# Optimization experiments

Hardware: AMD Instinct MI355X
Metric: run time of the kernel (lower is better)

The kernel has to match this reference:

```python
import jax, jax.numpy as jnp
import numpy as np

B, S, D = 2, 2048, 1024
H, DH = 16, 64  # n_heads, d_head; inner_dim = H*DH = 1024


def setup_inputs() -> dict:
    key = jax.random.key(0)
    ks = jax.random.split(key, 6)
    s = 0.02
    return {
        "query": jax.random.normal(ks[0], (B, S, D), jnp.float32),
        "context": jax.random.normal(ks[1], (B, S, D), jnp.float32),
        "Wq": jax.random.normal(ks[2], (D, H * DH), jnp.float32) * s,
        "Wk": jax.random.normal(ks[3], (D, H * DH), jnp.float32) * s,
        "Wv": jax.random.normal(ks[4], (D, H * DH), jnp.float32) * s,
        "Wo": jax.random.normal(ks[5], (H * DH, D), jnp.float32) * s,
        "bo": jnp.zeros((D,), jnp.float32),
    }


def reference(query, context, Wq, Wk, Wv, Wo, bo):
    scale = DH ** -0.5
    # projections -> [B, H, S, DH]
    q = (query @ Wq).reshape(B, S, H, DH).transpose(0, 2, 1, 3)
    k = (context @ Wk).reshape(B, S, H, DH).transpose(0, 2, 1, 3)
    v = (context @ Wv).reshape(B, S, H, DH).transpose(0, 2, 1, 3)
    scores = jnp.einsum("bhqd,bhkd->bhqk", q, k) * scale  # [B,H,S,S]
    probs = jax.nn.softmax(scores, axis=-1)
    out = jnp.einsum("bhqk,bhkd->bhqd", probs, v)  # [B,H,S,DH]
    out = out.transpose(0, 2, 1, 3).reshape(B, S, H * DH)
    return out @ Wo + bo
```

## Files before the change

### kernel.cpp

```cpp
#include <hip/hip_runtime.h>
#include <hip/hip_bf16.h>

typedef __attribute__((ext_vector_type(8))) short bf16x8;
typedef __attribute__((ext_vector_type(4))) float f32x4;
typedef __attribute__((ext_vector_type(16))) float f32x16;

#define B_ 2
#define S_ 2048
#define D_ 1024
#define H_ 16

__device__ __forceinline__ unsigned short f2bf(float x) {
  unsigned u = __float_as_uint(x);
  unsigned r = (u + 0x7fffu + ((u >> 16) & 1u)) >> 16;
  return (unsigned short)r;
}

__device__ __forceinline__ unsigned cvt_pk_bf16(float lo, float hi) {
  unsigned r;
  asm("v_cvt_pk_bf16_f32 %0, %1, %2" : "=v"(r) : "v"(lo), "v"(hi));
  return r;
}

__device__ __forceinline__ void gload_lds16(const void* g, void* l) {
  __builtin_amdgcn_global_load_lds((const __attribute__((address_space(1))) void*)g,
                                   (__attribute__((address_space(3))) void*)l, 16, 0, 0);
}

__global__ __launch_bounds__(256) void prep_kernel(const float* __restrict__ query,
                                                   const float* __restrict__ ctx,
                                                   const float* __restrict__ Wq, const float* __restrict__ Wk,
                                                   const float* __restrict__ Wv, const float* __restrict__ Wo,
                                                   unsigned short* __restrict__ qb, unsigned short* __restrict__ cb,
                                                   unsigned short* __restrict__ WqT, unsigned short* __restrict__ WkT,
                                                   unsigned short* __restrict__ WvT, unsigned short* __restrict__ WoT) {
  __shared__ float tile[32][33];
  int bid = blockIdx.x;
  if (bid < 8192) {
    const float* s = bid < 4096 ? query : ctx;
    unsigned short* d = bid < 4096 ? qb : cb;
    int i = (bid & 4095) * 256 + threadIdx.x;
    float4 v = ((const float4*)s)[i];
    ushort4 o;
    o.x = f2bf(v.x); o.y = f2bf(v.y); o.z = f2bf(v.z); o.w = f2bf(v.w);
    ((ushort4*)d)[i] = o;
    return;
  }
  int tid = bid - 8192;
  int z = tid >> 10, r = tid & 1023;
  const float* W; unsigned short* WT;
  if (z == 0)      { W = Wq; WT = WqT; }
  else if (z == 1) { W = Wk; WT = WkT; }
  else if (z == 2) { W = Wv; WT = WvT; }
  else             { W = Wo; WT = WoT; }
  int r0 = (r >> 5) * 32, c0 = (r & 31) * 32;
  int t = threadIdx.x;
  int lr = t >> 3, lc = (t & 7) * 4;
  float4 v = *(const float4*)&W[(size_t)(r0 + lr) * 1024 + c0 + lc];
  tile[lr][lc + 0] = v.x; tile[lr][lc + 1] = v.y; tile[lr][lc + 2] = v.z; tile[lr][lc + 3] = v.w;
  __syncthreads();
  ushort4 o;
  o.x = f2bf(tile[lc + 0][lr]);
  o.y = f2bf(tile[lc + 1][lr]);
  o.z = f2bf(tile[lc + 2][lr]);
  o.w = f2bf(tile[lc + 3][lr]);
  *(ushort4*)&WT[(size_t)(c0 + lr) * 1024 + r0 + lc] = o;
}

__device__ __forceinline__ void gemm_core(const unsigned short* __restrict__ A,
                                          const unsigned short* __restrict__ BT,
                                          int m0, int n0, int K,
                                          unsigned short* As, unsigned short* Bs,
                                          f32x4 (&acc)[4][4]) {
  const int t = threadIdx.x, w = t >> 6, l = t & 63;
  const int lr = l & 15, lg = (l >> 4) * 8;
  const int wm = (w >> 1) * 64, wn = (w & 1) * 64;

#define GSTAGE(buf, k0) do {                                                               \
    _Pragma("unroll")                                                                      \
    for (int it_ = 0; it_ < 2; ++it_) {                                                    \
      int o_ = t * 16 + it_ * 4096;                                                        \
      int row_ = o_ >> 6, ce_ = (o_ & 63) >> 1;                                            \
      gload_lds16(A + (size_t)(m0 + row_) * K + (k0) + ce_,                                \
                  (char*)As + (buf) * 8192 + it_ * 4096 + w * 1024);                       \
      gload_lds16(BT + (size_t)(n0 + row_) * K + (k0) + ce_,                               \
                  (char*)Bs + (buf) * 8192 + it_ * 4096 + w * 1024);                       \
    }                                                                                      \
  } while (0)

  GSTAGE(0, 0);
  __syncthreads();
  int cur = 0;
  const int NT = K >> 5;
  for (int kt = 0; kt < NT; ++kt) {
    if (kt < NT - 1) GSTAGE(cur ^ 1, (kt + 1) * 32);
    bf16x8 af[4], bfr[4];
#pragma unroll
    for (int mi = 0; mi < 4; ++mi) af[mi] = *(const bf16x8*)&As[cur * 4096 + (wm + mi * 16 + lr) * 32 + lg];
#pragma unroll
    for (int ni = 0; ni < 4; ++ni) bfr[ni] = *(const bf16x8*)&Bs[cur * 4096 + (wn + ni * 16 + lr) * 32 + lg];
    __builtin_amdgcn_s_setprio(1);
#pragma unroll
    for (int mi = 0; mi < 4; ++mi)
#pragma unroll
      for (int ni = 0; ni < 4; ++ni)
        acc[mi][ni] = __builtin_amdgcn_mfma_f32_16x16x32_bf16(af[mi], bfr[ni], acc[mi][ni], 0, 0, 0);
    __builtin_amdgcn_s_setprio(0);
    __syncthreads();
    cur ^= 1;
  }
#undef GSTAGE
}

__global__ __launch_bounds__(256) void gemm_qkv(const unsigned short* __restrict__ qb,
                                                const unsigned short* __restrict__ cb,
                                                const unsigned short* __restrict__ WqT,
                                                const unsigned short* __restrict__ WkT,
                                                const unsigned short* __restrict__ WvT,
                                                unsigned short* __restrict__ qp,
                                                unsigned short* __restrict__ kp,
                                                unsigned short* __restrict__ vt) {
  __shared__ unsigned short As[2 * 4096];
  __shared__ unsigned short Bs[2 * 4096];
  int wg = (blockIdx.x & 7) * 96 + (blockIdx.x >> 3);
  int z = wg >> 8, r = wg & 255;
  const unsigned short *A, *BT; unsigned short* C; int N, bx, by;
  float osc;
  if (z == 0)      { A = qb;  BT = WqT; C = qp; N = 1024; bx = r & 31; by = r >> 5; osc = 0.125f * 1.44269504089f; }
  else if (z == 1) { A = cb;  BT = WkT; C = kp; N = 1024; bx = r & 31; by = r >> 5; osc = 1.f; }
  else             { A = WvT; BT = cb;  C = vt; N = 4096; bx = r & 7;  by = r >> 3; osc = 1.f; }
  f32x4 acc[4][4];
#pragma unroll
  for (int mi = 0; mi < 4; ++mi)
#pragma unroll
    for (int ni = 0; ni < 4; ++ni) acc[mi][ni] = {0.f, 0.f, 0.f, 0.f};
  gemm_core(A, BT, bx * 128, by * 128, 1024, As, Bs, acc);
  const int t = threadIdx.x, w = t >> 6, l = t & 63;
  const int lr = l & 15, lg4 = (l >> 4) * 4;
  const int wm = (w >> 1) * 64, wn = (w & 1) * 64;
#pragma unroll
  for (int mi = 0; mi < 4; ++mi)
#pragma unroll
    for (int ni = 0; ni < 4; ++ni)
#pragma unroll
      for (int j = 0; j < 4; ++j)
        C[(size_t)(bx * 128 + wm + mi * 16 + lg4 + j) * N + by * 128 + wn + ni * 16 + lr] =
            f2bf(acc[mi][ni][j] * osc);
}

__global__ __launch_bounds__(256) void gemm_out(const unsigned short* __restrict__ A,
                                                const unsigned short* __restrict__ BT,
                                                const float* __restrict__ bias,
                                                float* __restrict__ C) {
  __shared__ unsigned short As[2 * 4096];
  __shared__ unsigned short Bs[2 * 4096];
  int wg = (blockIdx.x & 7) * 32 + (blockIdx.x >> 3);
  int bx = wg & 31, by = wg >> 5;
  f32x4 acc[4][4];
#pragma unroll
  for (int mi = 0; mi < 4; ++mi)
#pragma unroll
    for (int ni = 0; ni < 4; ++ni) acc[mi][ni] = {0.f, 0.f, 0.f, 0.f};
  gemm_core(A, BT, bx * 128, by * 128, 1024, As, Bs, acc);
  const int t = threadIdx.x, w = t >> 6, l = t & 63;
  const int lr = l & 15, lg4 = (l >> 4) * 4;
  const int wm = (w >> 1) * 64, wn = (w & 1) * 64;
#pragma unroll
  for (int mi = 0; mi < 4; ++mi)
#pragma unroll
    for (int ni = 0; ni < 4; ++ni) {
      int col = by * 128 + wn + ni * 16 + lr;
      float bv = bias[col];
#pragma unroll
      for (int j = 0; j < 4; ++j)
        C[(size_t)(bx * 128 + wm + mi * 16 + lg4 + j) * 1024 + col] = acc[mi][ni][j] + bv;
    }
}

__global__ __launch_bounds__(256) void attn_kernel(const unsigned short* __restrict__ Q,
                                                   const unsigned short* __restrict__ Kp,
                                                   const unsigned short* __restrict__ Vt,
                                                   unsigned short* __restrict__ O) {
  __shared__ char lds[32768];
  const int t = threadIdx.x, w = t >> 6, l = t & 63;
  const int l31 = l & 31, hi = l >> 5;
  const int nf = (blockIdx.x & 7) * 64 + (blockIdx.x >> 3);
  const int qt = nf & 15, h = (nf >> 4) & 15, b = nf >> 8;

  const int q = qt * 128 + w * 32 + l31;
  const size_t qbase = ((size_t)(b * S_ + q)) * 1024 + h * 64;
  bf16x8 qf[4];
#pragma unroll
  for (int c = 0; c < 4; ++c) qf[c] = *(const bf16x8*)&Q[qbase + c * 16 + hi * 8];

  const size_t kbase = (size_t)b * S_ * 1024 + h * 64;
  const size_t vtb = (size_t)(h * 64) * 4096 + (size_t)b * 2048;

  f32x16 oacc[2];
#pragma unroll
  for (int d = 0; d < 2; ++d)
#pragma unroll
    for (int r = 0; r < 16; ++r) oacc[d][r] = 0.f;
  float l_run = 0.f;

#define STAGE(bsel, kv0) do {                                                          \
    char* kdst = lds + (bsel) * 16384;                                                 \
    char* vdst = kdst + 8192;                                                          \
    _Pragma("unroll")                                                                  \
    for (int it_ = 0; it_ < 2; ++it_) {                                                \
      const int off_ = it_ * 4096 + w * 1024 + l * 16;                                 \
      const int row_ = off_ >> 7, cb_ = off_ & 127;                                    \
      const int sc_ = (cb_ ^ ((row_ & 7) << 4)) >> 1;                                  \
      gload_lds16(Kp + kbase + (size_t)((kv0) + row_) * 1024 + sc_,                    \
                  kdst + it_ * 4096 + w * 1024);                                       \
      gload_lds16(Vt + vtb + (size_t)row_ * 4096 + (kv0) + sc_,                        \
                  vdst + it_ * 4096 + w * 1024);                                       \
    }                                                                                  \
  } while (0)

  STAGE(0, 0);
  __syncthreads();
  int cur = 0;
  const int sw = (l & 7) << 4;

  for (int tile = 0; tile < 32; ++tile) {
    if (tile < 31) STAGE(cur ^ 1, (tile + 1) * 64);
    const char* kb = lds + cur * 16384;
    const char* vb = kb + 8192;

    f32x16 sacc[2];
#pragma unroll
    for (int kvb = 0; kvb < 2; ++kvb) {
#pragma unroll
      for (int r = 0; r < 16; ++r) sacc[kvb][r] = 0.f;
      const int row = kvb * 32 + l31;
      __builtin_amdgcn_s_setprio(1);
#pragma unroll
      for (int c = 0; c < 4; ++c) {
        bf16x8 kf = *(const bf16x8*)(kb + row * 128 + ((c * 32 + hi * 16) ^ sw));
        sacc[kvb] = __builtin_amdgcn_mfma_f32_32x32x16_bf16(kf, qf[c], sacc[kvb], 0, 0, 0);
      }
      __builtin_amdgcn_s_setprio(0);
    }

    float rs = 0.f;
#pragma unroll
    for (int kvb = 0; kvb < 2; ++kvb)
#pragma unroll
      for (int r = 0; r < 16; ++r) {
        float p = exp2f(sacc[kvb][r]);
        sacc[kvb][r] = p;
        rs += p;
      }
    rs += __shfl_xor(rs, 32, 64);
    l_run += rs;

#pragma unroll
    for (int c = 0; c < 4; ++c) {
      const int sb = c >> 1, r0 = (c & 1) * 8;
      unsigned wA = cvt_pk_bf16(sacc[sb][r0 + 0], sacc[sb][r0 + 1]);
      unsigned wB = cvt_pk_bf16(sacc[sb][r0 + 2], sacc[sb][r0 + 3]);
      unsigned wC = cvt_pk_bf16(sacc[sb][r0 + 4], sacc[sb][r0 + 5]);
      unsigned wD = cvt_pk_bf16(sacc[sb][r0 + 6], sacc[sb][r0 + 7]);
      unsigned s0 = hi ? wA : wC;
      unsigned s1 = hi ? wB : wD;
      unsigned x0 = (unsigned)__shfl_xor((int)s0, 32, 64);
      unsigned x1 = (unsigned)__shfl_xor((int)s1, 32, 64);
      union { unsigned u[4]; bf16x8 v; } pf;
      pf.u[0] = hi ? x0 : wA;
      pf.u[1] = hi ? x1 : wB;
      pf.u[2] = hi ? wC : x0;
      pf.u[3] = hi ? wD : x1;
      __builtin_amdgcn_s_setprio(1);
#pragma unroll
      for (int d = 0; d < 2; ++d) {
        const int vrow = d * 32 + l31;
        bf16x8 vf = *(const bf16x8*)(vb + vrow * 128 + ((c * 32 + hi * 16) ^ sw));
        oacc[d] = __builtin_amdgcn_mfma_f32_32x32x16_bf16(vf, pf.v, oacc[d], 0, 0, 0);
      }
      __builtin_amdgcn_s_setprio(0);
    }
    __syncthreads();
    cur ^= 1;
  }

  const float inv = 1.f / l_run;
#pragma unroll
  for (int d = 0; d < 2; ++d)
#pragma unroll
    for (int rg = 0; rg < 4; ++rg) {
      ushort4 o4;
      o4.x = f2bf(oacc[d][rg * 4 + 0] * inv);
      o4.y = f2bf(oacc[d][rg * 4 + 1] * inv);
      o4.z = f2bf(oacc[d][rg * 4 + 2] * inv);
      o4.w = f2bf(oacc[d][rg * 4 + 3] * inv);
      *(ushort4*)&O[qbase + d * 32 + rg * 8 + hi * 4] = o4;
    }
#undef STAGE
}

extern "C" void kernel_launch(void* const* d_in, const int* in_sizes, int n_in,
                              void* d_out, int out_size, void* d_ws, size_t ws_size,
                              hipStream_t stream) {
  const float* query   = (const float*)d_in[0];
  const float* context = (const float*)d_in[1];
  const float* Wq = (const float*)d_in[2];
  const float* Wk = (const float*)d_in[3];
  const float* Wv = (const float*)d_in[4];
  const float* Wo = (const float*)d_in[5];
  const float* bo = (const float*)d_in[6];
  float* out = (float*)d_out;

  const size_t NA = (size_t)B_ * S_ * D_;
  const size_t NW = (size_t)D_ * D_;
  unsigned short* ws  = (unsigned short*)d_ws;
  unsigned short* qb  = ws;
  unsigned short* cb  = qb + NA;
  unsigned short* WqT = cb + NA;
  unsigned short* WkT = WqT + NW;
  unsigned short* WvT = WkT + NW;
  unsigned short* WoT = WvT + NW;
  unsigned short* qp  = WoT + NW;
  unsigned short* kp  = qp + NA;
  unsigned short* vt  = kp + NA;
  unsigned short* ao  = qb;

  prep_kernel<<<12288, 256, 0, stream>>>(query, context, Wq, Wk, Wv, Wo,
                                         qb, cb, WqT, WkT, WvT, WoT);
  gemm_qkv<<<768, 256, 0, stream>>>(qb, cb, WqT, WkT, WvT, qp, kp, vt);
  attn_kernel<<<512, 256, 0, stream>>>(qp, kp, vt, ao);
  gemm_out<<<256, 256, 0, stream>>>(ao, WoT, bo, out);
}
```

Before: 148.4 us.

## Triple-buffer LDS staging with vmcnt-based barriers and split attention accumulators

The GEMM core and the attention kernel move from double-buffered to triple-buffered LDS staging. Loads are issued two tiles ahead, and each full __syncthreads is replaced by an s_waitcnt vmcnt(4) plus a bare barrier, so the load for the next tile stays in flight across the barrier. The attention kernel also splits the PV accumulator into two independent sets, which breaks the MFMA dependency chain; the sets are summed at the end. In exchange LDS use grows (GEMM 48KB, attention 48KB), which may lower occupancy, and the attention kernel holds 32 more accumulator VGPRs.

```diff
diff --git a/kernel.cpp b/kernel.cpp
--- a/kernel.cpp
+++ b/kernel.cpp
@@ -26,6 +26,12 @@
   __builtin_amdgcn_global_load_lds((const __attribute__((address_space(1))) void*)g,
                                    (__attribute__((address_space(3))) void*)l, 16, 0, 0);
 }
+
+#define VM_BARRIER(N) do {                                   \
+    asm volatile("s_waitcnt vmcnt(" #N ")" ::: "memory");    \
+    __builtin_amdgcn_s_barrier();                            \
+    __builtin_amdgcn_sched_barrier(0);                       \
+  } while (0)
 
 __global__ __launch_bounds__(256) void prep_kernel(const float* __restrict__ query,
                                                    const float* __restrict__ ctx,
@@ -69,12 +75,13 @@
 
 __device__ __forceinline__ void gemm_core(const unsigned short* __restrict__ A,
                                           const unsigned short* __restrict__ BT,
-                                          int m0, int n0, int K,
+                                          int m0, int n0,
                                           unsigned short* As, unsigned short* Bs,
                                           f32x4 (&acc)[4][4]) {
   const int t = threadIdx.x, w = t >> 6, l = t & 63;
   const int lr = l & 15, lg = (l >> 4) * 8;
   const int wm = (w >> 1) * 64, wn = (w & 1) * 64;
+  const int K = 1024;
 
 #define GSTAGE(buf, k0) do {                                                               \
     _Pragma("unroll")                                                                      \
@@ -89,11 +96,12 @@
   } while (0)
 
   GSTAGE(0, 0);
-  __syncthreads();
+  GSTAGE(1, 32);
+  VM_BARRIER(4);
   int cur = 0;
-  const int NT = K >> 5;
-  for (int kt = 0; kt < NT; ++kt) {
-    if (kt < NT - 1) GSTAGE(cur ^ 1, (kt + 1) * 32);
+  for (int kt = 0; kt < 32; ++kt) {
+    int nb = cur + 2; if (nb >= 3) nb -= 3;
+    if (kt < 30) GSTAGE(nb, (kt + 2) * 32);
     bf16x8 af[4], bfr[4];
 #pragma unroll
     for (int mi = 0; mi < 4; ++mi) af[mi] = *(const bf16x8*)&As[cur * 4096 + (wm + mi * 16 + lr) * 32 + lg];
@@ -106,8 +114,9 @@
       for (int ni = 0; ni < 4; ++ni)
         acc[mi][ni] = __builtin_amdgcn_mfma_f32_16x16x32_bf16(af[mi], bfr[ni], acc[mi][ni], 0, 0, 0);
     __builtin_amdgcn_s_setprio(0);
-    __syncthreads();
-    cur ^= 1;
+    if (kt < 30) VM_BARRIER(4);
+    else if (kt == 30) VM_BARRIER(0);
+    cur = (cur == 2) ? 0 : cur + 1;
   }
 #undef GSTAGE
 }
@@ -120,8 +129,8 @@
                                                 unsigned short* __restrict__ qp,
                                                 unsigned short* __restrict__ kp,
                                                 unsigned short* __restrict__ vt) {
-  __shared__ unsigned short As[2 * 4096];
-  __shared__ unsigned short Bs[2 * 4096];
+  __shared__ unsigned short As[3 * 4096];
+  __shared__ unsigned short Bs[3 * 4096];
   int wg = (blockIdx.x & 7) * 96 + (blockIdx.x >> 3);
   int z = wg >> 8, r = wg & 255;
   const unsigned short *A, *BT; unsigned short* C; int N, bx, by;
@@ -134,7 +143,7 @@
   for (int mi = 0; mi < 4; ++mi)
 #pragma unroll
     for (int ni = 0; ni < 4; ++ni) acc[mi][ni] = {0.f, 0.f, 0.f, 0.f};
-  gemm_core(A, BT, bx * 128, by * 128, 1024, As, Bs, acc);
+  gemm_core(A, BT, bx * 128, by * 128, As, Bs, acc);
   const int t = threadIdx.x, w = t >> 6, l = t & 63;
   const int lr = l & 15, lg4 = (l >> 4) * 4;
   const int wm = (w >> 1) * 64, wn = (w & 1) * 64;
@@ -152,8 +161,8 @@
                                                 const unsigned short* __restrict__ BT,
                                                 const float* __restrict__ bias,
                                                 float* __restrict__ C) {
-  __shared__ unsigned short As[2 * 4096];
-  __shared__ unsigned short Bs[2 * 4096];
+  __shared__ unsigned short As[3 * 4096];
+  __shared__ unsigned short Bs[3 * 4096];
   int wg = (blockIdx.x & 7) * 32 + (blockIdx.x >> 3);
   int bx = wg & 31, by = wg >> 5;
   f32x4 acc[4][4];
@@ -161,7 +170,7 @@
   for (int mi = 0; mi < 4; ++mi)
 #pragma unroll
     for (int ni = 0; ni < 4; ++ni) acc[mi][ni] = {0.f, 0.f, 0.f, 0.f};
-  gemm_core(A, BT, bx * 128, by * 128, 1024, As, Bs, acc);
+  gemm_core(A, BT, bx * 128, by * 128, As, Bs, acc);
   const int t = threadIdx.x, w = t >> 6, l = t & 63;
   const int lr = l & 15, lg4 = (l >> 4) * 4;
   const int wm = (w >> 1) * 64, wn = (w & 1) * 64;
@@ -181,7 +190,7 @@
                                                    const unsigned short* __restrict__ Kp,
                                                    const unsigned short* __restrict__ Vt,
                                                    unsigned short* __restrict__ O) {
-  __shared__ char lds[32768];
+  __shared__ char lds[49152];
   const int t = threadIdx.x, w = t >> 6, l = t & 63;
   const int l31 = l & 31, hi = l >> 5;
   const int nf = (blockIdx.x & 7) * 64 + (blockIdx.x >> 3);
@@ -196,11 +205,11 @@
   const size_t kbase = (size_t)b * S_ * 1024 + h * 64;
   const size_t vtb = (size_t)(h * 64) * 4096 + (size_t)b * 2048;
 
-  f32x16 oacc[2];
+  f32x16 oaccA[2], oaccB[2];
 #pragma unroll
   for (int d = 0; d < 2; ++d)
 #pragma unroll
-    for (int r = 0; r < 16; ++r) oacc[d][r] = 0.f;
+    for (int r = 0; r < 16; ++r) { oaccA[d][r] = 0.f; oaccB[d][r] = 0.f; }
   float l_run = 0.f;
 
 #define STAGE(bsel, kv0) do {                                                          \
@@ -219,12 +228,14 @@
   } while (0)
 
   STAGE(0, 0);
-  __syncthreads();
+  STAGE(1, 64);
+  VM_BARRIER(4);
   int cur = 0;
   const int sw = (l & 7) << 4;
 
   for (int tile = 0; tile < 32; ++tile) {
-    if (tile < 31) STAGE(cur ^ 1, (tile + 1) * 64);
+    int nb = cur + 2; if (nb >= 3) nb -= 3;
+    if (tile < 30) STAGE(nb, (tile + 2) * 64);
     const char* kb = lds + cur * 16384;
     const char* vb = kb + 8192;
 
@@ -276,12 +287,14 @@
       for (int d = 0; d < 2; ++d) {
         const int vrow = d * 32 + l31;
         bf16x8 vf = *(const bf16x8*)(vb + vrow * 128 + ((c * 32 + hi * 16) ^ sw));
-        oacc[d] = __builtin_amdgcn_mfma_f32_32x32x16_bf16(vf, pf.v, oacc[d], 0, 0, 0);
+        if (c & 1) oaccB[d] = __builtin_amdgcn_mfma_f32_32x32x16_bf16(vf, pf.v, oaccB[d], 0, 0, 0);
+        else       oaccA[d] = __builtin_amdgcn_mfma_f32_32x32x16_bf16(vf, pf.v, oaccA[d], 0, 0, 0);
       }
       __builtin_amdgcn_s_setprio(0);
     }
-    __syncthreads();
-    cur ^= 1;
+    if (tile < 30) VM_BARRIER(4);
+    else if (tile == 30) VM_BARRIER(0);
+    cur = (cur == 2) ? 0 : cur + 1;
   }
 
   const float inv = 1.f / l_run;
@@ -290,10 +303,10 @@
 #pragma unroll
     for (int rg = 0; rg < 4; ++rg) {
       ushort4 o4;
-      o4.x = f2bf(oacc[d][rg * 4 + 0] * inv);
-      o4.y = f2bf(oacc[d][rg * 4 + 1] * inv);
-      o4.z = f2bf(oacc[d][rg * 4 + 2] * inv);
-      o4.w = f2bf(oacc[d][rg * 4 + 3] * inv);
+      o4.x = f2bf((oaccA[d][rg * 4 + 0] + oaccB[d][rg * 4 + 0]) * inv);
+      o4.y = f2bf((oaccA[d][rg * 4 + 1] + oaccB[d][rg * 4 + 1]) * inv);
+      o4.z = f2bf((oaccA[d][rg * 4 + 2] + oaccB[d][rg * 4 + 2]) * inv);
+      o4.w = f2bf((oaccA[d][rg * 4 + 3] + oaccB[d][rg * 4 + 3]) * inv);
       *(ushort4*)&O[qbase + d * 32 + rg * 8 + hi * 4] = o4;
     }
 #undef STAGE
```

Measured after the change: 146.6 us. About the same (-1.3%).
